# Optimization experiments

Measured on AMD Instinct MI355X. Metric: run time of the kernel, lower is better.

## Reference

```python
import jax, jax.numpy as jnp
import numpy as np

N_SYM = 128
BATCH = 131072
LEVERAGE = 30.0


def setup_inputs() -> dict:
    key = jax.random.key(0)
    ks = jax.random.split(key, 8)
    fractions = jax.random.normal(ks[0], (N_SYM, BATCH), dtype=jnp.float32)
    # exec_samples are Bernoulli(0/1) execution indicators, kept as float
    exec_samples = jnp.round(jax.random.uniform(ks[1], (N_SYM, BATCH), dtype=jnp.float32))
    pos_sizes = jax.random.normal(ks[2], (N_SYM, BATCH), dtype=jnp.float32)
    # margin rates strictly positive
    margin_rates = jax.random.uniform(ks[3], (N_SYM, BATCH), dtype=jnp.float32) * 0.9 + 0.1
    unused_margin = jax.random.uniform(ks[4], (BATCH,), dtype=jnp.float32) * 1000.0
    # per-symbol volume constraints: min == step (typical broker config), max >> min
    msm_step = jax.random.uniform(ks[5], (N_SYM,), dtype=jnp.float32) * 0.01 + 0.01
    msm_min = msm_step
    msm_max = msm_step * 1000.0
    return {
        "fractions": fractions,
        "exec_samples": exec_samples,
        "pos_sizes": pos_sizes,
        "margin_rates": margin_rates,
        "unused_margin": unused_margin,
        "msm_min": msm_min,
        "msm_step": msm_step,
        "msm_max": msm_max,
    }


def reference(fractions, exec_samples, pos_sizes, margin_rates, unused_margin,
              msm_min, msm_step, msm_max):
    """JAX port of LowLevelInferenceEngine._compute_new_pos_sizes.

    Sequential recurrence over traded symbols (axis 0), carrying
    unused_margin [BATCH]. Returns (new_pos_sizes [N_SYM, BATCH],
    final unused_margin [BATCH]).
    """

    def step_fn(um, xs):
        frac, ex, pos, mr, mn, st, mx = xs
        unused_size = um * mr * LEVERAGE
        max_pos_size = jnp.abs(pos) + unused_size
        # torch.where(pos*frac > 0, unused_size, max_pos_size).minimum(0)
        adj = jnp.minimum(jnp.where(pos * frac > 0, unused_size, max_pos_size), 0.0)
        new_pos_size = frac * (max_pos_size - adj)
        abs_nps = jnp.abs(new_pos_size)
        sgn = jnp.sign(new_pos_size)
        abs_nps = jnp.floor(abs_nps / st) * st
        abs_nps = jnp.where(abs_nps < mn, 0.0, abs_nps)
        abs_nps = jnp.minimum(abs_nps, mx)
        out = ex * (sgn * abs_nps) + (1.0 - ex) * pos
        um_new = (max_pos_size - abs_nps) / (mr * LEVERAGE)
        return um_new, out

    um_final, new_pos_sizes = jax.lax.scan(
        step_fn,
        unused_margin,
        (fractions, exec_samples, pos_sizes, margin_rates, msm_min, msm_step, msm_max),
    )
    return new_pos_sizes, um_final
```

## Files before the change

### kernel.cpp

```cpp
#include <hip/hip_runtime.h>
#include <math.h>

#define N_SYM 128
#define BATCH 131072
#define LEV   30.0f

__global__ __launch_bounds__(256) void lle_scan_kernel(
    const float* __restrict__ frac,
    const float* __restrict__ exs,
    const float* __restrict__ pos,
    const float* __restrict__ mrate,
    const float* __restrict__ um0,
    const float* __restrict__ msm_min,
    const float* __restrict__ msm_step,
    const float* __restrict__ msm_max,
    float* __restrict__ out)
{
    const int col = blockIdx.x * blockDim.x + threadIdx.x;

    float um = um0[col];

    size_t idx = (size_t)col;
    float f = frac[idx];
    float e = exs[idx];
    float p = pos[idx];
    float m = mrate[idx];

#pragma unroll 4
    for (int s = 0; s < N_SYM; ++s) {
        const size_t nidx = idx + (size_t)BATCH;
        float fn = 0.0f, en = 0.0f, pn = 0.0f, mn2 = 0.0f;
        if (s + 1 < N_SYM) {
            fn  = frac[nidx];
            en  = exs[nidx];
            pn  = pos[nidx];
            mn2 = mrate[nidx];
        }

        const float mrl = m * LEV;
        const float us  = um * mrl;
        const float mps = fabsf(p) + us;
        const float adj = fminf((p * f > 0.0f) ? us : mps, 0.0f);
        const float nps = f * (mps - adj);

        float       a  = fabsf(nps);
        const float sg = copysignf(1.0f, nps);

        const float stp = msm_step[s];
        a = floorf(a / stp) * stp;
        a = (a < msm_min[s]) ? 0.0f : a;
        a = fminf(a, msm_max[s]);

        out[idx] = e * (sg * a) + (1.0f - e) * p;

        um = (mps - a) / mrl;

        f = fn; e = en; p = pn; m = mn2;
        idx = nidx;
    }

    out[(size_t)N_SYM * (size_t)BATCH + (size_t)col] = um;
}

extern "C" void kernel_launch(void* const* d_in, const int* in_sizes, int n_in,
                              void* d_out, int out_size, void* d_ws, size_t ws_size,
                              hipStream_t stream) {
    const float* frac     = (const float*)d_in[0];
    const float* exs      = (const float*)d_in[1];
    const float* pos      = (const float*)d_in[2];
    const float* mrate    = (const float*)d_in[3];
    const float* um0      = (const float*)d_in[4];
    const float* msm_min  = (const float*)d_in[5];
    const float* msm_step = (const float*)d_in[6];
    const float* msm_max  = (const float*)d_in[7];
    float* out = (float*)d_out;

    const int block = 256;
    const int grid  = BATCH / block;

    hipLaunchKernelGGL(lle_scan_kernel, dim3(grid), dim3(block), 0, stream,
                       frac, exs, pos, mrate, um0, msm_min, msm_step, msm_max,
                       out);
}
```

Baseline: 277.7 us.

## Deepen software prefetch to eight symbols ahead and use nontemporal stores

Replaces the single-step lookahead with a register ring buffer that keeps loads for eight future symbols in flight while the sequential recurrence runs. This puts more memory requests in flight per thread, hiding load latency on a memory-bound scan. Output stores become nontemporal so the write stream does not pollute cache. The ring buffer costs extra registers, which can lower occupancy.

```diff
diff --git a/kernel.cpp b/kernel.cpp
--- a/kernel.cpp
+++ b/kernel.cpp
@@ -4,6 +4,7 @@
 #define N_SYM 128
 #define BATCH 131072
 #define LEV   30.0f
+#define PF    8
 
 __global__ __launch_bounds__(256) void lle_scan_kernel(
     const float* __restrict__ frac,
@@ -20,22 +21,61 @@
 
     float um = um0[col];
 
-    size_t idx = (size_t)col;
-    float f = frac[idx];
-    float e = exs[idx];
-    float p = pos[idx];
-    float m = mrate[idx];
+    float fb[PF], eb[PF], pb[PF], mb[PF];
 
-#pragma unroll 4
-    for (int s = 0; s < N_SYM; ++s) {
-        const size_t nidx = idx + (size_t)BATCH;
-        float fn = 0.0f, en = 0.0f, pn = 0.0f, mn2 = 0.0f;
-        if (s + 1 < N_SYM) {
-            fn  = frac[nidx];
-            en  = exs[nidx];
-            pn  = pos[nidx];
-            mn2 = mrate[nidx];
+#pragma unroll
+    for (int j = 0; j < PF; ++j) {
+        const size_t o = (size_t)j * BATCH + (size_t)col;
+        fb[j] = frac[o];
+        eb[j] = exs[o];
+        pb[j] = pos[o];
+        mb[j] = mrate[o];
+    }
+
+    for (int s0 = 0; s0 < N_SYM - PF; s0 += PF) {
+#pragma unroll
+        for (int j = 0; j < PF; ++j) {
+            const int s = s0 + j;
+            const float f = fb[j];
+            const float e = eb[j];
+            const float p = pb[j];
+            const float m = mb[j];
+
+            {
+                const size_t o = (size_t)(s + PF) * BATCH + (size_t)col;
+                fb[j] = frac[o];
+                eb[j] = exs[o];
+                pb[j] = pos[o];
+                mb[j] = mrate[o];
+            }
+
+            const float mrl = m * LEV;
+            const float us  = um * mrl;
+            const float mps = fabsf(p) + us;
+            const float adj = fminf((p * f > 0.0f) ? us : mps, 0.0f);
+            const float nps = f * (mps - adj);
+
+            float       a  = fabsf(nps);
+            const float sg = copysignf(1.0f, nps);
+            const float st = msm_step[s];
+            a = floorf(a / st) * st;
+            a = (a < msm_min[s]) ? 0.0f : a;
+            a = fminf(a, msm_max[s]);
+
+            const float res = e * (sg * a) + (1.0f - e) * p;
+            __builtin_nontemporal_store(res, &out[(size_t)s * BATCH + (size_t)col]);
+
+            um = (mps - a) / mrl;
         }
+    }
+
+#pragma unroll
+    for (int j = 0; j < PF; ++j) {
+        const int s = N_SYM - PF + j;
+        const float f = fb[j];
+        const float e = eb[j];
+        const float p = pb[j];
+        const float m = mb[j];
 
         const float mrl = m * LEV;
         const float us  = um * mrl;
@@ -45,21 +85,18 @@
 
         float       a  = fabsf(nps);
         const float sg = copysignf(1.0f, nps);
-
-        const float stp = msm_step[s];
-        a = floorf(a / stp) * stp;
+        const float st = msm_step[s];
+        a = floorf(a / st) * st;
         a = (a < msm_min[s]) ? 0.0f : a;
         a = fminf(a, msm_max[s]);
 
-        out[idx] = e * (sg * a) + (1.0f - e) * p;
+        const float res = e * (sg * a) + (1.0f - e) * p;
+        __builtin_nontemporal_store(res, &out[(size_t)s * BATCH + (size_t)col]);
 
         um = (mps - a) / mrl;
-
-        f = fn; e = en; p = pn; m = mn2;
-        idx = nidx;
     }
 
-    out[(size_t)N_SYM * (size_t)BATCH + (size_t)col] = um;
+    __builtin_nontemporal_store(um, &out[(size_t)N_SYM * BATCH + (size_t)col]);
 }
 
 extern "C" void kernel_launch(void* const* d_in, const int* in_sizes, int n_in,
```

Result: no change. 275.9 us (-0.7%).

## Vectorize scan to float4 per thread with 4-deep register prefetch pipeline

Applied to the files above, without the earlier changes.

Each thread now processes four adjacent batch columns using 16-byte vector loads and stores, instead of one column with scalar accesses. A 4-step register ring buffer prefetches future symbol rows so more memory requests are in flight. Loads and stores are nontemporal, and blocks shrink to 64 threads. The aim is to raise effective memory-level parallelism in this bandwidth-bound recurrence. The trade-off is 4x fewer threads (lower occupancy) and higher register use.

```diff
diff --git a/kernel.cpp b/kernel.cpp
--- a/kernel.cpp
+++ b/kernel.cpp
@@ -3,9 +3,33 @@
 
 #define N_SYM 128
 #define BATCH 131072
+#define B4    (BATCH / 4)
 #define LEV   30.0f
+#define D     4
 
-__global__ __launch_bounds__(256) void lle_scan_kernel(
+typedef float v4 __attribute__((ext_vector_type(4)));
+
+__device__ __forceinline__ float step1(float f, float e, float p, float m,
+                                       float st, float mn, float mx,
+                                       float* um)
+{
+    const float mrl = m * LEV;
+    const float us  = *um * mrl;
+    const float mps = fabsf(p) + us;
+    const float adj = fminf((p * f > 0.0f) ? us : mps, 0.0f);
+    const float nps = f * (mps - adj);
+
+    float       a  = fabsf(nps);
+    const float sg = copysignf(1.0f, nps);
+    a = floorf(a / st) * st;
+    a = (a < mn) ? 0.0f : a;
+    a = fminf(a, mx);
+
+    *um = (mps - a) / mrl;
+    return e * (sg * a) + (1.0f - e) * p;
+}
+
+__global__ __launch_bounds__(64) void lle_scan_kernel(
     const float* __restrict__ frac,
     const float* __restrict__ exs,
     const float* __restrict__ pos,
@@ -16,50 +40,83 @@
     const float* __restrict__ msm_max,
     float* __restrict__ out)
 {
-    const int col = blockIdx.x * blockDim.x + threadIdx.x;
+    const size_t c4 = (size_t)(blockIdx.x * 64 + threadIdx.x);
 
-    float um = um0[col];
+    const v4* F = (const v4*)frac;
+    const v4* E = (const v4*)exs;
+    const v4* P = (const v4*)pos;
+    const v4* M = (const v4*)mrate;
+    v4*       O = (v4*)out;
 
-    size_t idx = (size_t)col;
-    float f = frac[idx];
-    float e = exs[idx];
-    float p = pos[idx];
-    float m = mrate[idx];
+    const v4 umv = __builtin_nontemporal_load((const v4*)um0 + c4);
+    float um[4] = {umv.x, umv.y, umv.z, umv.w};
 
-#pragma unroll 4
-    for (int s = 0; s < N_SYM; ++s) {
-        const size_t nidx = idx + (size_t)BATCH;
-        float fn = 0.0f, en = 0.0f, pn = 0.0f, mn2 = 0.0f;
-        if (s + 1 < N_SYM) {
-            fn  = frac[nidx];
-            en  = exs[nidx];
-            pn  = pos[nidx];
-            mn2 = mrate[nidx];
-        }
+    v4 fb[D], eb[D], pb[D], mb[D];
 
-        const float mrl = m * LEV;
-        const float us  = um * mrl;
-        const float mps = fabsf(p) + us;
-        const float adj = fminf((p * f > 0.0f) ? us : mps, 0.0f);
-        const float nps = f * (mps - adj);
-
-        float       a  = fabsf(nps);
-        const float sg = copysignf(1.0f, nps);
-
-        const float stp = msm_step[s];
-        a = floorf(a / stp) * stp;
-        a = (a < msm_min[s]) ? 0.0f : a;
-        a = fminf(a, msm_max[s]);
-
-        out[idx] = e * (sg * a) + (1.0f - e) * p;
-
-        um = (mps - a) / mrl;
-
-        f = fn; e = en; p = pn; m = mn2;
-        idx = nidx;
+#pragma unroll
+    for (int j = 0; j < D; ++j) {
+        const size_t o = (size_t)j * B4 + c4;
+        fb[j] = __builtin_nontemporal_load(F + o);
+        eb[j] = __builtin_nontemporal_load(E + o);
+        pb[j] = __builtin_nontemporal_load(P + o);
+        mb[j] = __builtin_nontemporal_load(M + o);
     }
 
-    out[(size_t)N_SYM * (size_t)BATCH + (size_t)col] = um;
+    for (int s0 = 0; s0 < N_SYM - D; s0 += D) {
+#pragma unroll
+        for (int j = 0; j < D; ++j) {
+            const int s = s0 + j;
+            const v4 f = fb[j];
+            const v4 e = eb[j];
+            const v4 p = pb[j];
+            const v4 m = mb[j];
+
+            {
+                const size_t o = (size_t)(s + D) * B4 + c4;
+                fb[j] = __builtin_nontemporal_load(F + o);
+                eb[j] = __builtin_nontemporal_load(E + o);
+                pb[j] = __builtin_nontemporal_load(P + o);
+                mb[j] = __builtin_nontemporal_load(M + o);
+            }
+
+            const float st = msm_step[s];
+            const float mn = msm_min[s];
+            const float mx = msm_max[s];
+
+            v4 r;
+            r.x = step1(f.x, e.x, p.x, m.x, st, mn, mx, &um[0]);
+            r.y = step1(f.y, e.y, p.y, m.y, st, mn, mx, &um[1]);
+            r.z = step1(f.z, e.z, p.z, m.z, st, mn, mx, &um[2]);
+            r.w = step1(f.w, e.w, p.w, m.w, st, mn, mx, &um[3]);
+
+            __builtin_nontemporal_store(r, O + (size_t)s * B4 + c4);
+        }
+    }
+
+#pragma unroll
+    for (int j = 0; j < D; ++j) {
+        const int s = N_SYM - D + j;
+        const v4 f = fb[j];
+        const v4 e = eb[j];
+        const v4 p = pb[j];
+        const v4 m = mb[j];
+
+        const float st = msm_step[s];
+        const float mn = msm_min[s];
+        const float mx = msm_max[s];
+
+        v4 r;
+        r.x = step1(f.x, e.x, p.x, m.x, st, mn, mx, &um[0]);
+        r.y = step1(f.y, e.y, p.y, m.y, st, mn, mx, &um[1]);
+        r.z = step1(f.z, e.z, p.z, m.z, st, mn, mx, &um[2]);
+        r.w = step1(f.w, e.w, p.w, m.w, st, mn, mx, &um[3]);
+
+        __builtin_nontemporal_store(r, O + (size_t)s * B4 + c4);
+    }
+
+    v4 umo;
+    umo.x = um[0]; umo.y = um[1]; umo.z = um[2]; umo.w = um[3];
+    __builtin_nontemporal_store(umo, O + (size_t)N_SYM * B4 + c4);
 }
 
 extern "C" void kernel_launch(void* const* d_in, const int* in_sizes, int n_in,
@@ -75,8 +132,8 @@
     const float* msm_max  = (const float*)d_in[7];
     float* out = (float*)d_out;
 
-    const int block = 256;
-    const int grid  = BATCH / block;
+    const int block = 64;
+    const int grid  = (BATCH / 4) / block;
 
     hipLaunchKernelGGL(lle_scan_kernel, dim3(grid), dim3(block), 0, stream,
                        frac, exs, pos, mrate, um0, msm_min, msm_step, msm_max,
```

Measured after the change: 257.8 us. 1.08x faster.
